# Performance work log

Measured on AMD Instinct MI355X. Metric: run time of the kernel, lower is better.

The kernel has to match this reference:

```python
import jax, jax.numpy as jnp
import numpy as np

HEADS = 16
DIM_HEAD = 128
DIM = HEADS * DIM_HEAD          # hidden_size = 2048
SEGMENT_LEN = 496
NUM_LONGTERM = 16
NUM_PERSIST = 16
C = SEGMENT_LEN + NUM_LONGTERM  # total_segment_len = 512 (window width)
EPS = 1e-6
THETA = 10000.0
NEG = -jnp.finfo(jnp.float32).max


def _rope(t, cos, sin):
    # t: [b, h, n, d]; cos/sin: [n, d]; interleaved (rotate-half on adjacent pairs)
    t2 = t.reshape(t.shape[:-1] + (DIM_HEAD // 2, 2))
    rot = jnp.stack((-t2[..., 1], t2[..., 0]), axis=-1).reshape(t.shape)
    return t * cos + rot * sin


def _attn_bias():
    # queries: [m_len longterm-mem tokens | segment tokens]
    # keys:    [p_len persistent | m_len longterm-mem | segment tokens]
    q_len = C
    k_len = C + NUM_PERSIST
    pq = NUM_LONGTERM
    pk = NUM_PERSIST + NUM_LONGTERM
    bias = jnp.full((q_len, k_len), NEG, dtype=jnp.float32)
    bias = bias.at[:, :pk].set(0.0)  # everyone attends to the prefix
    sq = q_len - pq
    causal = jnp.tril(jnp.ones((sq, sq), dtype=bool))
    bias = bias.at[pq:, pk:].set(jnp.where(causal, 0.0, NEG))
    return bias


def setup_inputs() -> dict:
    key = jax.random.key(0)
    k1, k2, k3, k4 = jax.random.split(key, 4)
    b, n = 2, 4096  # n must be a multiple of C=512
    return {
        "x": jax.random.normal(k1, (b, n, DIM), dtype=jnp.float32),
        "norm_w": jnp.ones((DIM,), dtype=jnp.float32),
        "w_qkv": jax.random.normal(k2, (3 * DIM, DIM), dtype=jnp.float32) * 0.02,
        "w_out": jax.random.normal(k3, (DIM, DIM), dtype=jnp.float32) * 0.02,
        "pm": jax.random.normal(k4, (2, HEADS, NUM_PERSIST, DIM_HEAD), dtype=jnp.float32) * 0.02,
    }


def reference(x, norm_w, w_qkv, w_out, pm):
    b, n, d = x.shape
    # RMSNorm
    xn = x * jax.lax.rsqrt(jnp.mean(x * x, axis=-1, keepdims=True) + EPS) * norm_w
    # qkv projection (Linear, no bias)
    qkv = xn @ w_qkv.T
    q, k, v = jnp.split(qkv, 3, axis=-1)

    def to_heads(t):  # [b, n, h*d] -> [b, h, n, d]
        return t.reshape(b, n, HEADS, DIM_HEAD).transpose(0, 2, 1, 3)

    q, k, v = to_heads(q), to_heads(k), to_heads(v)

    # RoPE over full sequence positions 0..n-1 (before windowing)
    inv_freq = 1.0 / (THETA ** (jnp.arange(0, DIM_HEAD, 2, dtype=jnp.float32) / DIM_HEAD))
    freqs = jnp.arange(n, dtype=jnp.float32)[:, None] * inv_freq  # [n, d/2]
    freqs = jnp.repeat(freqs, 2, axis=-1)                          # [n, d]
    cos, sin = jnp.cos(freqs), jnp.sin(freqs)
    q = _rope(q, cos, sin)
    k = _rope(k, cos, sin)

    # split into windows of width C: [b, h, n, d] -> [(b*w), h, C, d]
    w = n // C

    def to_windows(t):
        return t.reshape(b, HEADS, w, C, DIM_HEAD).transpose(0, 2, 1, 3, 4).reshape(b * w, HEADS, C, DIM_HEAD)

    q, k, v = to_windows(q), to_windows(k), to_windows(v)

    # prepend persistent memory tokens to k, v
    pmk = jnp.broadcast_to(pm[0], (b * w, HEADS, NUM_PERSIST, DIM_HEAD))
    pmv = jnp.broadcast_to(pm[1], (b * w, HEADS, NUM_PERSIST, DIM_HEAD))
    k = jnp.concatenate((pmk, k), axis=-2)  # [(b*w), h, C+P, d]
    v = jnp.concatenate((pmv, v), axis=-2)

    bias = _attn_bias()  # [C, C+P]
    scale = DIM_HEAD ** -0.5
    sim = jnp.einsum('whqd,whkd->whqk', q, k) * scale + bias
    attn = jax.nn.softmax(sim, axis=-1)
    out = jnp.einsum('whqk,whkd->whqd', attn, v)

    # '(b w) h c d -> b (w c) (h d)'
    out = out.reshape(b, w, HEADS, C, DIM_HEAD).transpose(0, 1, 3, 2, 4).reshape(b, n, HEADS * DIM_HEAD)
    return out @ w_out.T
```

## Files before the change

### kernel.cpp

```cpp
#include <hip/hip_runtime.h>
#include <hip/hip_bf16.h>

typedef __attribute__((ext_vector_type(8))) short short8v;
typedef __attribute__((ext_vector_type(4))) float f32x4;
typedef __attribute__((ext_vector_type(4))) unsigned short us4;

#define DEV static __device__ __forceinline__

DEV unsigned short f2bf(float f) {
  unsigned u = __builtin_bit_cast(unsigned, f);
  u += 0x7FFFu + ((u >> 16) & 1u);
  return (unsigned short)(u >> 16);
}
DEV float bf2f(unsigned short s) {
  unsigned u = ((unsigned)s) << 16;
  return __builtin_bit_cast(float, u);
}
DEV void gload16(const void* g, void* l) {
  __builtin_amdgcn_global_load_lds((const __attribute__((address_space(1))) void*)g,
                                   (__attribute__((address_space(3))) void*)l, 16, 0, 0);
}

__global__ __launch_bounds__(256) void k_cvt(const float* __restrict__ s,
                                             unsigned short* __restrict__ d, long n4) {
  long i = (long)blockIdx.x * 256 + threadIdx.x;
  if (i >= n4) return;
  f32x4 v = *((const f32x4*)s + i);
  us4 o;
  o[0] = f2bf(v[0]); o[1] = f2bf(v[1]); o[2] = f2bf(v[2]); o[3] = f2bf(v[3]);
  *((us4*)d + i) = o;
}

__global__ __launch_bounds__(256) void k_pmprep(const float* __restrict__ pm,
                                                unsigned short* __restrict__ pmk,
                                                unsigned short* __restrict__ vt,
                                                unsigned short* __restrict__ zbuf) {
  int idx = blockIdx.x * 256 + threadIdx.x;
  if (idx < 8) zbuf[idx] = 0;
  if (idx >= 16 * 16 * 128) return;
  int d = idx & 127, p = (idx >> 7) & 15, h = idx >> 11;
  float kvl = pm[((0 * 16 + h) * 16 + p) * 128 + d];
  float vvl = pm[((1 * 16 + h) * 16 + p) * 128 + d];
  pmk[(h * 16 + p) * 128 + d] = f2bf(kvl);
  unsigned short vb = f2bf(vvl);
  for (int w = 0; w < 16; ++w) {
    long base = ((long)(w * 16 + h) * 128 + d) * 544;
    vt[base + p] = vb;
    vt[base + 528 + p] = 0;
  }
}

__global__ __launch_bounds__(256) void k_ropetab(float* __restrict__ ct, float* __restrict__ st) {
  int idx = blockIdx.x * 256 + threadIdx.x;
  int pos = idx >> 6, i = idx & 63;
  float invf = __powf(10000.f, -(float)i * (1.f / 64.f));
  float a = (float)pos * invf;
  ct[idx] = cosf(a);
  st[idx] = sinf(a);
}

__global__ __launch_bounds__(256) void k_rms(const float* __restrict__ x,
                                             const float* __restrict__ w,
                                             unsigned short* __restrict__ xb) {
  int row = blockIdx.x, tid = threadIdx.x;
  const f32x4* xr = (const f32x4*)(x + (long)row * 2048);
  f32x4 v0 = xr[tid * 2], v1 = xr[tid * 2 + 1];
  float ss = v0[0]*v0[0] + v0[1]*v0[1] + v0[2]*v0[2] + v0[3]*v0[3]
           + v1[0]*v1[0] + v1[1]*v1[1] + v1[2]*v1[2] + v1[3]*v1[3];
  ss += __shfl_xor(ss, 1);  ss += __shfl_xor(ss, 2);  ss += __shfl_xor(ss, 4);
  ss += __shfl_xor(ss, 8);  ss += __shfl_xor(ss, 16); ss += __shfl_xor(ss, 32);
  __shared__ float red[4];
  if ((tid & 63) == 0) red[tid >> 6] = ss;
  __syncthreads();
  float tot = red[0] + red[1] + red[2] + red[3];
  float rs = rsqrtf(tot * (1.f / 2048.f) + 1e-6f);
  float xv[8] = {v0[0], v0[1], v0[2], v0[3], v1[0], v1[1], v1[2], v1[3]};
  short8v pack;
#pragma unroll
  for (int j = 0; j < 8; ++j) pack[j] = (short)f2bf(xv[j] * rs * w[tid * 8 + j]);
  *((short8v*)(xb + (long)row * 2048) + tid) = pack;
}


#define VMCNT4 asm volatile("s_waitcnt vmcnt(4)" ::: "memory")
#define VMCNT0 asm volatile("s_waitcnt vmcnt(0)" ::: "memory")
#define SCHEDB __builtin_amdgcn_sched_barrier(0)
#define NOSTG ((void)0)

template <int OUTF32>
__global__ __launch_bounds__(512, 2) void k_gemm8(const unsigned short* __restrict__ A,
                                                  const unsigned short* __restrict__ B,
                                                  unsigned short* __restrict__ Cb,
                                                  float* __restrict__ Cf,
                                                  int M, int N, int K) {
  __shared__ __align__(16) unsigned short lds[4 * 256 * 64];
  const int tid = threadIdx.x;
  const int lane = tid & 63;
  const int ql = lane & 15, g = lane >> 4;
  const int wid = tid >> 6;
  const int wm = wid >> 2, wn = wid & 3;

  const int nbx = N >> 8;
  const int nwg = gridDim.x;
  int bid = blockIdx.x;
  int swz = (bid & 7) * (nwg >> 3) + (bid >> 3);
  int by = swz / nbx, bx = swz - by * nbx;
  const long rowA0 = (long)by << 8;
  const long rowB0 = (long)bx << 8;

  const int idx0 = tid, idx1 = 512 + tid;
  const int dr0 = idx0 >> 3, sc0 = (idx0 & 7) ^ (dr0 & 7);
  const int dr1 = idx1 >> 3, sc1 = (idx1 & 7) ^ (dr1 & 7);
  const long halfA = 128L * K;
  const unsigned short* pA0 = A + (rowA0 + dr0) * (long)K + sc0 * 8;
  const unsigned short* pA1 = A + (rowA0 + dr1) * (long)K + sc1 * 8;
  const unsigned short* pB0 = B + (rowB0 + dr0) * (long)K + sc0 * 8;
  const unsigned short* pB1 = B + (rowB0 + dr1) * (long)K + sc1 * 8;

  const int rsw0 = (g ^ (ql & 7)) * 8;
  const int rsw1 = ((4 + g) ^ (ql & 7)) * 8;

  short8v fa[4], fb[2][4];
  f32x4 acc[8][4] = {};

#define STAGE_A(b, h, kk) do { \
  gload16(pA0 + (long)(h) * halfA + (kk), lds + (b) * 32768 + (h) * 8192 + (idx0 << 3)); \
  gload16(pA1 + (long)(h) * halfA + (kk), lds + (b) * 32768 + (h) * 8192 + (idx1 << 3)); } while (0)
#define STAGE_B(b, h, kk) do { \
  gload16(pB0 + (long)(h) * halfA + (kk), lds + (b) * 32768 + 16384 + (h) * 8192 + (idx0 << 3)); \
  gload16(pB1 + (long)(h) * halfA + (kk), lds + (b) * 32768 + 16384 + (h) * 8192 + (idx1 << 3)); } while (0)

#define PHASE(buf, mh, ks, LOADB, STG, VMC) do { \
  { const unsigned short* p_ = lds + (buf) * 32768 + (((wm << 7) + (mh) * 64 + ql) << 6) + ((ks) ? rsw1 : rsw0); \
    _Pragma("unroll") for (int mi_ = 0; mi_ < 4; ++mi_) fa[mi_] = *(const short8v*)(p_ + (mi_ << 10)); } \
  if (LOADB) { const unsigned short* p_ = lds + (buf) * 32768 + 16384 + (((wn << 6) + ql) << 6) + ((ks) ? rsw1 : rsw0); \
    _Pragma("unroll") for (int n_ = 0; n_ < 4; ++n_) fb[ks][n_] = *(const short8v*)(p_ + (n_ << 10)); } \
  STG; \
  SCHEDB; __builtin_amdgcn_s_barrier(); SCHEDB; \
  __builtin_amdgcn_s_setprio(1); \
  _Pragma("unroll") for (int mi_ = 0; mi_ < 4; ++mi_) \
    _Pragma("unroll") for (int n_ = 0; n_ < 4; ++n_) \
      acc[(mh) * 4 + mi_][n_] = __builtin_amdgcn_mfma_f32_16x16x32_bf16(fa[mi_], fb[ks][n_], acc[(mh) * 4 + mi_][n_], 0, 0, 0); \
  __builtin_amdgcn_s_setprio(0); \
  VMC; \
  SCHEDB; __builtin_amdgcn_s_barrier(); SCHEDB; \
} while (0)

  const int NT = K >> 6;
  const int NITER = NT >> 1;

  STAGE_A(0, 0, 0); STAGE_A(0, 1, 0);
  STAGE_B(0, 0, 0); STAGE_B(0, 1, 0);
  STAGE_B(1, 0, 64); STAGE_B(1, 1, 64);
  VMCNT4;
  SCHEDB; __builtin_amdgcn_s_barrier(); SCHEDB;

  for (int i = 0; i < NITER - 1; ++i) {
    const int k1 = (2 * i + 1) << 6;
    const int k2 = (2 * i + 2) << 6;
    const int k3 = (2 * i + 3) << 6;
    PHASE(0, 0, 0, 1, STAGE_A(1, 0, k1), NOSTG);
    PHASE(0, 0, 1, 1, STAGE_A(1, 1, k1), NOSTG);
    PHASE(0, 1, 0, 0, STAGE_B(0, 0, k2), NOSTG);
    PHASE(0, 1, 1, 0, STAGE_B(0, 1, k2), VMCNT4);
    PHASE(1, 0, 0, 1, STAGE_A(0, 0, k2), NOSTG);
    PHASE(1, 0, 1, 1, STAGE_A(0, 1, k2), NOSTG);
    PHASE(1, 1, 0, 0, STAGE_B(1, 0, k3), NOSTG);
    PHASE(1, 1, 1, 0, STAGE_B(1, 1, k3), VMCNT4);
  }
  {
    const int k1 = (NT - 1) << 6;
    PHASE(0, 0, 0, 1, STAGE_A(1, 0, k1), NOSTG);
    PHASE(0, 0, 1, 1, STAGE_A(1, 1, k1), NOSTG);
    PHASE(0, 1, 0, 0, NOSTG, NOSTG);
    PHASE(0, 1, 1, 0, NOSTG, VMCNT0);
    PHASE(1, 0, 0, 1, NOSTG, NOSTG);
    PHASE(1, 0, 1, 1, NOSTG, NOSTG);
    PHASE(1, 1, 0, 0, NOSTG, NOSTG);
    PHASE(1, 1, 1, 0, NOSTG, NOSTG);
  }

#pragma unroll
  for (int am = 0; am < 8; ++am)
#pragma unroll
    for (int n = 0; n < 4; ++n)
#pragma unroll
      for (int r = 0; r < 4; ++r) {
        long row = rowA0 + (wm << 7) + am * 16 + (g << 2) + r;
        long col = rowB0 + (wn << 6) + n * 16 + ql;
        if (OUTF32) Cf[row * N + col] = acc[am][n][r];
        else        Cb[row * N + col] = f2bf(acc[am][n][r]);
      }
#undef STAGE_A
#undef STAGE_B
#undef PHASE
}

__global__ __launch_bounds__(256) void k_rope(unsigned short* __restrict__ qkv,
                                              const float* __restrict__ ct,
                                              const float* __restrict__ st) {
  long idx = (long)blockIdx.x * 256 + threadIdx.x;
  if (idx >= 8388608L) return;
  int t = (int)(idx >> 10);
  int h = (int)((idx >> 6) & 15);
  int i = (int)(idx & 63);
  int pos = t & 4095;
  float c = ct[pos * 64 + i], s = st[pos * 64 + i];
  long qoff = (long)t * 6144 + h * 128 + 2 * i;
  unsigned q01 = *(const unsigned*)(qkv + qoff);
  float a = bf2f((unsigned short)(q01 & 0xffff)), b = bf2f((unsigned short)(q01 >> 16));
  const float SC = 0.08838834764831845f;
  float ra = (a * c - b * s) * SC, rb = (b * c + a * s) * SC;
  *(unsigned*)(qkv + qoff) = (unsigned)f2bf(ra) | ((unsigned)f2bf(rb) << 16);
  long koff = qoff + 2048;
  unsigned k01 = *(const unsigned*)(qkv + koff);
  a = bf2f((unsigned short)(k01 & 0xffff)); b = bf2f((unsigned short)(k01 >> 16));
  ra = a * c - b * s; rb = b * c + a * s;
  *(unsigned*)(qkv + koff) = (unsigned)f2bf(ra) | ((unsigned)f2bf(rb) << 16);
}

__global__ __launch_bounds__(256) void k_vtb(const unsigned short* __restrict__ qkv,
                                             unsigned short* __restrict__ vt) {
  __shared__ unsigned short lt[64 * 136];
  int tile = blockIdx.x, h = blockIdx.y;
  int tid = threadIdx.x;
  int t0 = tile * 64;
  {
    int row = tid >> 2, seg = tid & 3;
    const unsigned short* src = qkv + (long)(t0 + row) * 6144 + 4096 + h * 128 + seg * 32;
#pragma unroll
    for (int j = 0; j < 4; ++j)
      *(short8v*)(lt + row * 136 + seg * 32 + j * 8) = *(const short8v*)(src + j * 8);
  }
  __syncthreads();
  int d = tid >> 1, half = tid & 1;
  int wh = t0 >> 9;
  long dst = ((long)(wh * 16 + h) * 128 + d) * 544 + (t0 & 511) + 16 + half * 32;
  unsigned short tmp[32];
#pragma unroll
  for (int kk = 0; kk < 32; ++kk) tmp[kk] = lt[(half * 32 + kk) * 136 + d];
#pragma unroll
  for (int j = 0; j < 4; ++j) {
    short8v v;
#pragma unroll
    for (int e = 0; e < 8; ++e) v[e] = (short)tmp[j * 8 + e];
    *(short8v*)(vt + dst + j * 8) = v;
  }
}

__global__ __launch_bounds__(256) void k_attn(const unsigned short* __restrict__ qkv,
                                              const unsigned short* __restrict__ vt,
                                              const unsigned short* __restrict__ pmk,
                                              const unsigned short* __restrict__ zbuf,
                                              unsigned short* __restrict__ attno) {
  __shared__ __align__(16) unsigned short Ks[32 * 128];
  __shared__ __align__(16) unsigned short Vs[128 * 32];
  const int qb = blockIdx.x, wh = blockIdx.y, h = blockIdx.z;
  const int tid = threadIdx.x;
  const int wave = tid >> 6, lane = tid & 63;
  const int ql = lane & 15, g = lane >> 4;
  const int tokbase = (wh >> 3) * 4096 + (wh & 7) * 512;
  const int qi = qb * 64 + wave * 16 + ql;
  const long qrow = (long)(tokbase + qi) * 6144;
  short8v qf[4];
#pragma unroll
  for (int ks = 0; ks < 4; ++ks)
    qf[ks] = *(const short8v*)(qkv + qrow + h * 128 + ks * 32 + g * 8);
  float mrun = -3.0e38f, lrun = 0.f;
  f32x4 o[8] = {};
  const int nkt = min(17, (qb * 64 + 64 + 16 + 31) >> 5);
  const long vbase = ((long)(wh * 16 + h) * 128) * 544;
  for (int kt = 0; kt < nkt; ++kt) {
#pragma unroll
    for (int i = 0; i < 2; ++i) {
      int c = i * 256 + tid;
      int kl = c >> 4, dc = c & 15;
      int dcs = dc ^ (kl & 7);
      int ki = kt * 32 + kl;
      const unsigned short* src;
      if (ki < 16)       src = pmk + (h * 16 + ki) * 128 + dcs * 8;
      else if (ki < 528) src = qkv + (long)(tokbase + ki - 16) * 6144 + 2048 + h * 128 + dcs * 8;
      else               src = zbuf;
      gload16(src, Ks + (size_t)(i * 256 + wave * 64) * 8);
    }
#pragma unroll
    for (int i = 0; i < 2; ++i) {
      int c = i * 256 + tid;
      int d = c >> 2, kc = c & 3;
      int kcs = kc ^ (d & 3);
      gload16(vt + vbase + (long)d * 544 + kt * 32 + kcs * 8, Vs + (size_t)(i * 256 + wave * 64) * 8);
    }
    __syncthreads();
    f32x4 st[2] = {};
#pragma unroll
    for (int kf = 0; kf < 2; ++kf) {
      int row = kf * 16 + ql;
#pragma unroll
      for (int ks = 0; ks < 4; ++ks) {
        int dchunk = (ks * 4 + g) ^ (row & 7);
        short8v kv = *(const short8v*)(Ks + row * 128 + dchunk * 8);
        st[kf] = __builtin_amdgcn_mfma_f32_16x16x32_bf16(kv, qf[ks], st[kf], 0, 0, 0);
      }
    }
    float tmax = -3.0e38f;
#pragma unroll
    for (int kf = 0; kf < 2; ++kf)
#pragma unroll
      for (int r = 0; r < 4; ++r) {
        int ki = kt * 32 + kf * 16 + g * 4 + r;
        bool ok = (ki < 32) || (qi >= 16 && ki <= qi + 16);
        float s = ok ? st[kf][r] : -3.0e38f;
        st[kf][r] = s;
        tmax = fmaxf(tmax, s);
      }
    tmax = fmaxf(tmax, __shfl_xor(tmax, 16));
    tmax = fmaxf(tmax, __shfl_xor(tmax, 32));
    float mnew = fmaxf(mrun, tmax);
    float corr = __expf(mrun - mnew);
    float psum = 0.f;
#pragma unroll
    for (int kf = 0; kf < 2; ++kf)
#pragma unroll
      for (int r = 0; r < 4; ++r) {
        float p = __expf(st[kf][r] - mnew);
        st[kf][r] = p;
        psum += p;
      }
    psum += __shfl_xor(psum, 16);
    psum += __shfl_xor(psum, 32);
    lrun = lrun * corr + psum;
    mrun = mnew;
#pragma unroll
    for (int db = 0; db < 8; ++db) {
      o[db][0] *= corr; o[db][1] *= corr; o[db][2] *= corr; o[db][3] *= corr;
    }
    short8v pb;
#pragma unroll
    for (int j = 0; j < 8; ++j) {
      int srcl = ((((g & 1) * 2 + (j >> 2))) << 4) | ql;
      float v0 = __shfl(st[0][j & 3], srcl);
      float v1 = __shfl(st[1][j & 3], srcl);
      pb[j] = (short)f2bf((g >> 1) ? v1 : v0);
    }
#pragma unroll
    for (int db = 0; db < 8; ++db) {
      int d = db * 16 + ql;
      int kc = g ^ (d & 3);
      short8v vf = *(const short8v*)(Vs + d * 32 + kc * 8);
      o[db] = __builtin_amdgcn_mfma_f32_16x16x32_bf16(vf, pb, o[db], 0, 0, 0);
    }
    __syncthreads();
  }
  float inv = 1.0f / lrun;
  long obase = (long)(tokbase + qi) * 2048 + h * 128;
#pragma unroll
  for (int db = 0; db < 8; ++db)
#pragma unroll
    for (int r = 0; r < 4; ++r)
      attno[obase + db * 16 + g * 4 + r] = f2bf(o[db][r] * inv);
}

extern "C" void kernel_launch(void* const* d_in, const int* in_sizes, int n_in,
                              void* d_out, int out_size, void* d_ws, size_t ws_size,
                              hipStream_t stream) {
  const float* x      = (const float*)d_in[0];
  const float* norm_w = (const float*)d_in[1];
  const float* w_qkv  = (const float*)d_in[2];
  const float* w_out  = (const float*)d_in[3];
  const float* pm     = (const float*)d_in[4];
  float* out = (float*)d_out;

  char* ws = (char*)d_ws;
  size_t off = 0;
  auto alloc = [&](size_t bytes) -> void* {
    void* p = ws + off;
    off += (bytes + 255) & ~(size_t)255;
    return p;
  };
  unsigned short* xb    = (unsigned short*)alloc(8192ull * 2048 * 2);
  unsigned short* wqkvb = (unsigned short*)alloc(6144ull * 2048 * 2);
  unsigned short* woutb = (unsigned short*)alloc(2048ull * 2048 * 2);
  unsigned short* qkv   = (unsigned short*)alloc(8192ull * 6144 * 2);
  unsigned short* vt    = (unsigned short*)alloc(256ull * 128 * 544 * 2);
  unsigned short* attno = (unsigned short*)alloc(8192ull * 2048 * 2);
  unsigned short* pmk   = (unsigned short*)alloc(16 * 16 * 128 * 2);
  float* ct             = (float*)alloc(4096 * 64 * 4);
  float* stt            = (float*)alloc(4096 * 64 * 4);
  unsigned short* zbuf  = (unsigned short*)alloc(256);

  hipLaunchKernelGGL(k_cvt, dim3(12288), dim3(256), 0, stream, w_qkv, wqkvb, 3145728L);
  hipLaunchKernelGGL(k_cvt, dim3(4096), dim3(256), 0, stream, w_out, woutb, 1048576L);
  hipLaunchKernelGGL(k_pmprep, dim3(128), dim3(256), 0, stream, pm, pmk, vt, zbuf);
  hipLaunchKernelGGL(k_ropetab, dim3(1024), dim3(256), 0, stream, ct, stt);
  hipLaunchKernelGGL(k_rms, dim3(8192), dim3(256), 0, stream, x, norm_w, xb);
  hipLaunchKernelGGL((k_gemm8<0>), dim3(24 * 32), dim3(512), 0, stream,
                     xb, wqkvb, qkv, (float*)nullptr, 8192, 6144, 2048);
  hipLaunchKernelGGL(k_rope, dim3(32768), dim3(256), 0, stream, qkv, ct, stt);
  hipLaunchKernelGGL(k_vtb, dim3(128, 16), dim3(256), 0, stream, qkv, vt);
  hipLaunchKernelGGL(k_attn, dim3(8, 16, 16), dim3(256), 0, stream, qkv, vt, pmk, zbuf, attno);
  hipLaunchKernelGGL((k_gemm8<1>), dim3(8 * 32), dim3(512), 0, stream,
                     attno, woutb, (unsigned short*)nullptr, out, 8192, 2048, 2048);
}
```

Measured before the change: 448.1 us.

## Fuse RoPE into QKV GEMM, use 32x32 MFMA, rework attention tiling

```diff
diff --git a/kernel.cpp b/kernel.cpp
--- a/kernel.cpp
+++ b/kernel.cpp
@@ -3,6 +3,7 @@
 
 typedef __attribute__((ext_vector_type(8))) short short8v;
 typedef __attribute__((ext_vector_type(4))) float f32x4;
+typedef __attribute__((ext_vector_type(16))) float f32x16;
 typedef __attribute__((ext_vector_type(4))) unsigned short us4;
 
 #define DEV static __device__ __forceinline__
@@ -44,9 +45,11 @@
   pmk[(h * 16 + p) * 128 + d] = f2bf(kvl);
   unsigned short vb = f2bf(vvl);
   for (int w = 0; w < 16; ++w) {
-    long base = ((long)(w * 16 + h) * 128 + d) * 544;
+    long base = ((long)(w * 16 + h) * 128 + d) * 576;
     vt[base + p] = vb;
     vt[base + 528 + p] = 0;
+    vt[base + 544 + p] = 0;
+    vt[base + 560 + p] = 0;
   }
 }
 
@@ -87,16 +90,18 @@
 #define SCHEDB __builtin_amdgcn_sched_barrier(0)
 #define NOSTG ((void)0)
 
-template <int OUTF32>
+template <int OUTF32, int ROPE>
 __global__ __launch_bounds__(512, 2) void k_gemm8(const unsigned short* __restrict__ A,
                                                   const unsigned short* __restrict__ B,
                                                   unsigned short* __restrict__ Cb,
                                                   float* __restrict__ Cf,
+                                                  const float* __restrict__ ct,
+                                                  const float* __restrict__ stt,
                                                   int M, int N, int K) {
   __shared__ __align__(16) unsigned short lds[4 * 256 * 64];
   const int tid = threadIdx.x;
   const int lane = tid & 63;
-  const int ql = lane & 15, g = lane >> 4;
+  const int al = lane & 31, h8 = lane >> 5;
   const int wid = tid >> 6;
   const int wm = wid >> 2, wn = wid & 3;
 
@@ -117,11 +122,8 @@
   const unsigned short* pB0 = B + (rowB0 + dr0) * (long)K + sc0 * 8;
   const unsigned short* pB1 = B + (rowB0 + dr1) * (long)K + sc1 * 8;
 
-  const int rsw0 = (g ^ (ql & 7)) * 8;
-  const int rsw1 = ((4 + g) ^ (ql & 7)) * 8;
-
-  short8v fa[4], fb[2][4];
-  f32x4 acc[8][4] = {};
+  short8v fa[4], fb[2][2][2];
+  f32x16 acc[4][2] = {};
 
 #define STAGE_A(b, h, kk) do { \
   gload16(pA0 + (long)(h) * halfA + (kk), lds + (b) * 32768 + (h) * 8192 + (idx0 << 3)); \
@@ -130,17 +132,26 @@
   gload16(pB0 + (long)(h) * halfA + (kk), lds + (b) * 32768 + 16384 + (h) * 8192 + (idx0 << 3)); \
   gload16(pB1 + (long)(h) * halfA + (kk), lds + (b) * 32768 + 16384 + (h) * 8192 + (idx1 << 3)); } while (0)
 
-#define PHASE(buf, mh, ks, LOADB, STG, VMC) do { \
-  { const unsigned short* p_ = lds + (buf) * 32768 + (((wm << 7) + (mh) * 64 + ql) << 6) + ((ks) ? rsw1 : rsw0); \
-    _Pragma("unroll") for (int mi_ = 0; mi_ < 4; ++mi_) fa[mi_] = *(const short8v*)(p_ + (mi_ << 10)); } \
-  if (LOADB) { const unsigned short* p_ = lds + (buf) * 32768 + 16384 + (((wn << 6) + ql) << 6) + ((ks) ? rsw1 : rsw0); \
-    _Pragma("unroll") for (int n_ = 0; n_ < 4; ++n_) fb[ks][n_] = *(const short8v*)(p_ + (n_ << 10)); } \
+#define PHASE(buf, mh, kh, LOADB, STG, VMC) do { \
+  _Pragma("unroll") for (int t2_ = 0; t2_ < 2; ++t2_) \
+    _Pragma("unroll") for (int ks_ = 0; ks_ < 2; ++ks_) \
+      fa[t2_ * 2 + ks_] = *(const short8v*)(lds + (buf) * 32768 + \
+        (((wm << 7) + ((mh) * 2 + t2_) * 32 + al) << 6) + \
+        (((((kh) * 2 + ks_) * 2 + h8) ^ (al & 7)) << 3)); \
+  if (LOADB) { \
+    _Pragma("unroll") for (int tn_ = 0; tn_ < 2; ++tn_) \
+      _Pragma("unroll") for (int ks_ = 0; ks_ < 2; ++ks_) \
+        fb[kh][tn_][ks_] = *(const short8v*)(lds + (buf) * 32768 + 16384 + \
+          (((wn << 6) + tn_ * 32 + al) << 6) + \
+          (((((kh) * 2 + ks_) * 2 + h8) ^ (al & 7)) << 3)); } \
   STG; \
   SCHEDB; __builtin_amdgcn_s_barrier(); SCHEDB; \
   __builtin_amdgcn_s_setprio(1); \
-  _Pragma("unroll") for (int mi_ = 0; mi_ < 4; ++mi_) \
-    _Pragma("unroll") for (int n_ = 0; n_ < 4; ++n_) \
-      acc[(mh) * 4 + mi_][n_] = __builtin_amdgcn_mfma_f32_16x16x32_bf16(fa[mi_], fb[ks][n_], acc[(mh) * 4 + mi_][n_], 0, 0, 0); \
+  _Pragma("unroll") for (int t2_ = 0; t2_ < 2; ++t2_) \
+    _Pragma("unroll") for (int tn_ = 0; tn_ < 2; ++tn_) \
+      _Pragma("unroll") for (int ks_ = 0; ks_ < 2; ++ks_) \
+        acc[(mh) * 2 + t2_][tn_] = __builtin_amdgcn_mfma_f32_32x32x16_bf16( \
+            fa[t2_ * 2 + ks_], fb[kh][tn_][ks_], acc[(mh) * 2 + t2_][tn_], 0, 0, 0); \
   __builtin_amdgcn_s_setprio(0); \
   VMC; \
   SCHEDB; __builtin_amdgcn_s_barrier(); SCHEDB; \
@@ -181,42 +192,40 @@
   }
 
 #pragma unroll
-  for (int am = 0; am < 8; ++am)
-#pragma unroll
-    for (int n = 0; n < 4; ++n)
-#pragma unroll
-      for (int r = 0; r < 4; ++r) {
-        long row = rowA0 + (wm << 7) + am * 16 + (g << 2) + r;
-        long col = rowB0 + (wn << 6) + n * 16 + ql;
-        if (OUTF32) Cf[row * N + col] = acc[am][n][r];
-        else        Cb[row * N + col] = f2bf(acc[am][n][r]);
-      }
+  for (int tm = 0; tm < 4; ++tm)
+#pragma unroll
+    for (int tn = 0; tn < 2; ++tn) {
+      const int col = (int)rowB0 + (wn << 6) + tn * 32 + al;
+      if (ROPE) {
+        const bool isq = col < 2048;
+        const bool isqk = col < 4096;
+        const int ii = (col & 127) >> 1;
+        const int oddc = col & 1;
+#pragma unroll
+        for (int r = 0; r < 16; ++r) {
+          long row = rowA0 + (wm << 7) + tm * 32 + (r & 3) + ((r >> 2) << 3) + (h8 << 2);
+          float v = acc[tm][tn][r];
+          float other = __shfl_xor(v, 1);
+          if (isqk) {
+            int pos = (int)row & 4095;
+            float c = ct[pos * 64 + ii], s = stt[pos * 64 + ii];
+            v = oddc ? (v * c + other * s) : (v * c - other * s);
+            if (isq) v *= 0.08838834764831845f;
+          }
+          Cb[row * (long)N + col] = f2bf(v);
+        }
+      } else {
+#pragma unroll
+        for (int r = 0; r < 16; ++r) {
+          long row = rowA0 + (wm << 7) + tm * 32 + (r & 3) + ((r >> 2) << 3) + (h8 << 2);
+          if (OUTF32) Cf[row * (long)N + col] = acc[tm][tn][r];
+          else        Cb[row * (long)N + col] = f2bf(acc[tm][tn][r]);
+        }
+      }
+    }
 #undef STAGE_A
 #undef STAGE_B
 #undef PHASE
-}
-
-__global__ __launch_bounds__(256) void k_rope(unsigned short* __restrict__ qkv,
-                                              const float* __restrict__ ct,
-                                              const float* __restrict__ st) {
-  long idx = (long)blockIdx.x * 256 + threadIdx.x;
-  if (idx >= 8388608L) return;
-  int t = (int)(idx >> 10);
-  int h = (int)((idx >> 6) & 15);
-  int i = (int)(idx & 63);
-  int pos = t & 4095;
-  float c = ct[pos * 64 + i], s = st[pos * 64 + i];
-  long qoff = (long)t * 6144 + h * 128 + 2 * i;
-  unsigned q01 = *(const unsigned*)(qkv + qoff);
-  float a = bf2f((unsigned short)(q01 & 0xffff)), b = bf2f((unsigned short)(q01 >> 16));
-  const float SC = 0.08838834764831845f;
-  float ra = (a * c - b * s) * SC, rb = (b * c + a * s) * SC;
-  *(unsigned*)(qkv + qoff) = (unsigned)f2bf(ra) | ((unsigned)f2bf(rb) << 16);
-  long koff = qoff + 2048;
-  unsigned k01 = *(const unsigned*)(qkv + koff);
-  a = bf2f((unsigned short)(k01 & 0xffff)); b = bf2f((unsigned short)(k01 >> 16));
-  ra = a * c - b * s; rb = b * c + a * s;
-  *(unsigned*)(qkv + koff) = (unsigned)f2bf(ra) | ((unsigned)f2bf(rb) << 16);
 }
 
 __global__ __launch_bounds__(256) void k_vtb(const unsigned short* __restrict__ qkv,
@@ -235,7 +244,7 @@
   __syncthreads();
   int d = tid >> 1, half = tid & 1;
   int wh = t0 >> 9;
-  long dst = ((long)(wh * 16 + h) * 128 + d) * 544 + (t0 & 511) + 16 + half * 32;
+  long dst = ((long)(wh * 16 + h) * 128 + d) * 576 + (t0 & 511) + 16 + half * 32;
   unsigned short tmp[32];
 #pragma unroll
   for (int kk = 0; kk < 32; ++kk) tmp[kk] = lt[(half * 32 + kk) * 136 + d];
@@ -253,8 +262,7 @@
                                               const unsigned short* __restrict__ pmk,
                                               const unsigned short* __restrict__ zbuf,
                                               unsigned short* __restrict__ attno) {
-  __shared__ __align__(16) unsigned short Ks[32 * 128];
-  __shared__ __align__(16) unsigned short Vs[128 * 32];
+  __shared__ __align__(16) unsigned short Ks[2][64 * 128];
   const int qb = blockIdx.x, wh = blockIdx.y, h = blockIdx.z;
   const int tid = threadIdx.x;
   const int wave = tid >> 6, lane = tid & 63;
@@ -266,91 +274,98 @@
 #pragma unroll
   for (int ks = 0; ks < 4; ++ks)
     qf[ks] = *(const short8v*)(qkv + qrow + h * 128 + ks * 32 + g * 8);
+  const int nkt = min(9, (qb * 64 + 80 + 63) >> 6);
+  const long vbase = (long)(wh * 16 + h) * 128 * 576;
+
   float mrun = -3.0e38f, lrun = 0.f;
   f32x4 o[8] = {};
-  const int nkt = min(17, (qb * 64 + 64 + 16 + 31) >> 5);
-  const long vbase = ((long)(wh * 16 + h) * 128) * 544;
+
+#define STAGEK(kt, b) do { \
+  _Pragma("unroll") for (int i2 = 0; i2 < 4; ++i2) { \
+    int c_ = i2 * 256 + tid; \
+    int kl_ = c_ >> 4, dc_ = c_ & 15, dcs_ = dc_ ^ (kl_ & 7); \
+    int ki_ = (kt) * 64 + kl_; \
+    const unsigned short* src_; \
+    if (ki_ < 16)       src_ = pmk + (h * 16 + ki_) * 128 + dcs_ * 8; \
+    else if (ki_ < 528) src_ = qkv + (long)(tokbase + ki_ - 16) * 6144 + 2048 + h * 128 + dcs_ * 8; \
+    else                src_ = zbuf; \
+    gload16(src_, &Ks[b][0] + (size_t)c_ * 8); \
+  } } while (0)
+
+  STAGEK(0, 0);
+  __syncthreads();
   for (int kt = 0; kt < nkt; ++kt) {
-#pragma unroll
-    for (int i = 0; i < 2; ++i) {
-      int c = i * 256 + tid;
-      int kl = c >> 4, dc = c & 15;
-      int dcs = dc ^ (kl & 7);
-      int ki = kt * 32 + kl;
-      const unsigned short* src;
-      if (ki < 16)       src = pmk + (h * 16 + ki) * 128 + dcs * 8;
-      else if (ki < 528) src = qkv + (long)(tokbase + ki - 16) * 6144 + 2048 + h * 128 + dcs * 8;
-      else               src = zbuf;
-      gload16(src, Ks + (size_t)(i * 256 + wave * 64) * 8);
+    const int cur = kt & 1;
+    if (kt + 1 < nkt) { if (cur) STAGEK(kt + 1, 0); else STAGEK(kt + 1, 1); }
+    f32x4 stv[4] = {};
+#pragma unroll
+    for (int kf = 0; kf < 4; ++kf) {
+      int row = kf * 16 + ql;
+#pragma unroll
+      for (int ks = 0; ks < 4; ++ks) {
+        int chunk = (ks * 4 + g) ^ (row & 7);
+        short8v kv = *(const short8v*)(&Ks[cur][0] + row * 128 + chunk * 8);
+        stv[kf] = __builtin_amdgcn_mfma_f32_16x16x32_bf16(kv, qf[ks], stv[kf], 0, 0, 0);
+      }
     }
-#pragma unroll
-    for (int i = 0; i < 2; ++i) {
-      int c = i * 256 + tid;
-      int d = c >> 2, kc = c & 3;
-      int kcs = kc ^ (d & 3);
-      gload16(vt + vbase + (long)d * 544 + kt * 32 + kcs * 8, Vs + (size_t)(i * 256 + wave * 64) * 8);
+    float tmax = -3.0e38f;
+#pragma unroll
+    for (int kf = 0; kf < 4; ++kf)
+#pragma unroll
+      for (int r = 0; r < 4; ++r) {
+        int ki = kt * 64 + kf * 16 + g * 4 + r;
+        bool ok = (ki < 32) || (qi >= 16 && ki <= qi + 16);
+        float s = ok ? stv[kf][r] : -3.0e38f;
+        stv[kf][r] = s;
+        tmax = fmaxf(tmax, s);
+      }
+    tmax = fmaxf(tmax, __shfl_xor(tmax, 16));
+    tmax = fmaxf(tmax, __shfl_xor(tmax, 32));
+    if (!__all(tmax <= mrun + 8.f)) {
+      float mnew = fmaxf(mrun, tmax);
+      float corr = __expf(mrun - mnew);
+      lrun *= corr;
+#pragma unroll
+      for (int db = 0; db < 8; ++db) {
+        o[db][0] *= corr; o[db][1] *= corr; o[db][2] *= corr; o[db][3] *= corr;
+      }
+      mrun = mnew;
+    }
+    float psum = 0.f;
+#pragma unroll
+    for (int kf = 0; kf < 4; ++kf)
+#pragma unroll
+      for (int r = 0; r < 4; ++r) {
+        float p = __expf(stv[kf][r] - mrun);
+        stv[kf][r] = p;
+        psum += p;
+      }
+    psum += __shfl_xor(psum, 16);
+    psum += __shfl_xor(psum, 32);
+    lrun += psum;
+    short8v pb[2];
+#pragma unroll
+    for (int kc2 = 0; kc2 < 2; ++kc2)
+#pragma unroll
+      for (int j = 0; j < 8; ++j) {
+        int srcl = (((g & 1) * 2 + (j >> 2)) << 4) | ql;
+        float v0 = __shfl(stv[kc2 * 2][j & 3], srcl);
+        float v1 = __shfl(stv[kc2 * 2 + 1][j & 3], srcl);
+        pb[kc2][j] = (short)f2bf((g >> 1) ? v1 : v0);
+      }
+#pragma unroll
+    for (int db = 0; db < 8; ++db) {
+      int d = db * 16 + ql;
+      const unsigned short* vr = vt + vbase + (long)d * 576 + kt * 64;
+#pragma unroll
+      for (int kc2 = 0; kc2 < 2; ++kc2) {
+        short8v vf = *(const short8v*)(vr + kc2 * 32 + g * 8);
+        o[db] = __builtin_amdgcn_mfma_f32_16x16x32_bf16(vf, pb[kc2], o[db], 0, 0, 0);
+      }
     }
     __syncthreads();
-    f32x4 st[2] = {};
-#pragma unroll
-    for (int kf = 0; kf < 2; ++kf) {
-      int row = kf * 16 + ql;
-#pragma unroll
-      for (int ks = 0; ks < 4; ++ks) {
-        int dchunk = (ks * 4 + g) ^ (row & 7);
-        short8v kv = *(const short8v*)(Ks + row * 128 + dchunk * 8);
-        st[kf] = __builtin_amdgcn_mfma_f32_16x16x32_bf16(kv, qf[ks], st[kf], 0, 0, 0);
-      }
-    }
-    float tmax = -3.0e38f;
-#pragma unroll
-    for (int kf = 0; kf < 2; ++kf)
-#pragma unroll
-      for (int r = 0; r < 4; ++r) {
-        int ki = kt * 32 + kf * 16 + g * 4 + r;
-        bool ok = (ki < 32) || (qi >= 16 && ki <= qi + 16);
-        float s = ok ? st[kf][r] : -3.0e38f;
-        st[kf][r] = s;
-        tmax = fmaxf(tmax, s);
-      }
-    tmax = fmaxf(tmax, __shfl_xor(tmax, 16));
-    tmax = fmaxf(tmax, __shfl_xor(tmax, 32));
-    float mnew = fmaxf(mrun, tmax);
-    float corr = __expf(mrun - mnew);
-    float psum = 0.f;
-#pragma unroll
-    for (int kf = 0; kf < 2; ++kf)
-#pragma unroll
-      for (int r = 0; r < 4; ++r) {
-        float p = __expf(st[kf][r] - mnew);
-        st[kf][r] = p;
-        psum += p;
-      }
-    psum += __shfl_xor(psum, 16);
-    psum += __shfl_xor(psum, 32);
-    lrun = lrun * corr + psum;
-    mrun = mnew;
-#pragma unroll
-    for (int db = 0; db < 8; ++db) {
-      o[db][0] *= corr; o[db][1] *= corr; o[db][2] *= corr; o[db][3] *= corr;
-    }
-    short8v pb;
-#pragma unroll
-    for (int j = 0; j < 8; ++j) {
-      int srcl = ((((g & 1) * 2 + (j >> 2))) << 4) | ql;
-      float v0 = __shfl(st[0][j & 3], srcl);
-      float v1 = __shfl(st[1][j & 3], srcl);
-      pb[j] = (short)f2bf((g >> 1) ? v1 : v0);
-    }
-#pragma unroll
-    for (int db = 0; db < 8; ++db) {
-      int d = db * 16 + ql;
-      int kc = g ^ (d & 3);
-      short8v vf = *(const short8v*)(Vs + d * 32 + kc * 8);
-      o[db] = __builtin_amdgcn_mfma_f32_16x16x32_bf16(vf, pb, o[db], 0, 0, 0);
-    }
-    __syncthreads();
-  }
+  }
+#undef STAGEK
   float inv = 1.0f / lrun;
   long obase = (long)(tokbase + qi) * 2048 + h * 128;
 #pragma unroll
@@ -381,7 +396,7 @@
   unsigned short* wqkvb = (unsigned short*)alloc(6144ull * 2048 * 2);
   unsigned short* woutb = (unsigned short*)alloc(2048ull * 2048 * 2);
   unsigned short* qkv   = (unsigned short*)alloc(8192ull * 6144 * 2);
-  unsigned short* vt    = (unsigned short*)alloc(256ull * 128 * 544 * 2);
+  unsigned short* vt    = (unsigned short*)alloc(256ull * 128 * 576 * 2);
   unsigned short* attno = (unsigned short*)alloc(8192ull * 2048 * 2);
   unsigned short* pmk   = (unsigned short*)alloc(16 * 16 * 128 * 2);
   float* ct             = (float*)alloc(4096 * 64 * 4);
@@ -393,11 +408,10 @@
   hipLaunchKernelGGL(k_pmprep, dim3(128), dim3(256), 0, stream, pm, pmk, vt, zbuf);
   hipLaunchKernelGGL(k_ropetab, dim3(1024), dim3(256), 0, stream, ct, stt);
   hipLaunchKernelGGL(k_rms, dim3(8192), dim3(256), 0, stream, x, norm_w, xb);
-  hipLaunchKernelGGL((k_gemm8<0>), dim3(24 * 32), dim3(512), 0, stream,
-                     xb, wqkvb, qkv, (float*)nullptr, 8192, 6144, 2048);
-  hipLaunchKernelGGL(k_rope, dim3(32768), dim3(256), 0, stream, qkv, ct, stt);
+  hipLaunchKernelGGL((k_gemm8<0, 1>), dim3(24 * 32), dim3(512), 0, stream,
+                     xb, wqkvb, qkv, (float*)nullptr, ct, stt, 8192, 6144, 2048);
   hipLaunchKernelGGL(k_vtb, dim3(128, 16), dim3(256), 0, stream, qkv, vt);
   hipLaunchKernelGGL(k_attn, dim3(8, 16, 16), dim3(256), 0, stream, qkv, vt, pmk, zbuf, attno);
-  hipLaunchKernelGGL((k_gemm8<1>), dim3(8 * 32), dim3(512), 0, stream,
-                     attno, woutb, (unsigned short*)nullptr, out, 8192, 2048, 2048);
-}
+  hipLaunchKernelGGL((k_gemm8<1, 0>), dim3(8 * 32), dim3(512), 0, stream,
+                     attno, woutb, (unsigned short*)nullptr, out, ct, stt, 8192, 2048, 2048);
+}
```

After: 580.9 us. 1.3x slower.
